# Optimization experiments

Hardware: AMD Instinct MI355X
Metric: run time of the kernel (lower is better)

The kernel has to match this reference:

```python
import jax, jax.numpy as jnp
import numpy as np

B, S, D, H = 128, 256, 256, 8   # graphs, nodes/graph, dim_h, heads
N = B * S
E = 524288
DH = D // H
BN_EPS = 1e-5

def _bn(v, g, b):
    # BatchNorm1d forward with batch statistics (biased var), eval-dropout model
    m = v.mean(0)
    var = v.var(0)
    return (v - m) * jax.lax.rsqrt(var + BN_EPS) * g + b

def setup_inputs() -> dict:
    key = jax.random.key(0)
    ks = jax.random.split(key, 40)
    x = jax.random.normal(ks[0], (N, D), jnp.float32)
    src = jax.random.randint(ks[1], (E,), 0, N)
    dst = (src // S) * S + jax.random.randint(ks[2], (E,), 0, S)  # intra-graph edges
    edge_index = jnp.stack([src, dst]).astype(jnp.int64)
    def lin(k, i, o):
        return (jax.random.normal(k, (i, o), jnp.float32) / np.float32(np.sqrt(i)))
    inp = {
        'x': x, 'edge_index': edge_index,
        'W_gcn': lin(ks[3], D, D), 'b_gcn': jnp.zeros((D,), jnp.float32),
        'W_gin1': lin(ks[4], D, D), 'b_gin1': jnp.zeros((D,), jnp.float32),
        'W_gin2': lin(ks[5], D, D), 'b_gin2': jnp.zeros((D,), jnp.float32),
        'g_kv': jnp.ones((D,), jnp.float32), 'be_kv': jnp.zeros((D,), jnp.float32),
        'Wq1': lin(ks[6], D, D), 'bq1': jnp.zeros((D,), jnp.float32),
        'Wq2': lin(ks[7], D, D), 'bq2': jnp.zeros((D,), jnp.float32),
        'Wq_a': lin(ks[8], D, D), 'bq_a': jnp.zeros((D,), jnp.float32),
        'Wk_a': lin(ks[9], D, D), 'bk_a': jnp.zeros((D,), jnp.float32),
        'Wv_a': lin(ks[10], D, D), 'bv_a': jnp.zeros((D,), jnp.float32),
        'Wo_a': lin(ks[11], D, D), 'bo_a': jnp.zeros((D,), jnp.float32),
        'g_attn': jnp.ones((D,), jnp.float32), 'be_attn': jnp.zeros((D,), jnp.float32),
        'Wf1': lin(ks[12], D, 2 * D), 'bf1': jnp.zeros((2 * D,), jnp.float32),
        'Wf2': lin(ks[13], 2 * D, D), 'bf2': jnp.zeros((D,), jnp.float32),
        'g2': jnp.ones((D,), jnp.float32), 'be2': jnp.zeros((D,), jnp.float32),
    }
    return inp

def _forward(x, edge_index,
             W_gcn, b_gcn, W_gin1, b_gin1, W_gin2, b_gin2, g_kv, be_kv,
             Wq1, bq1, Wq2, bq2,
             Wq_a, bq_a, Wk_a, bk_a, Wv_a, bv_a, Wo_a, bo_a, g_attn, be_attn,
             Wf1, bf1, Wf2, bf2, g2, be2):
    row, col = edge_index[0], edge_index[1]
    h_in1 = x

    # ---- expert 0: GCNConv (add self loops + symmetric norm) ----
    loops = jnp.arange(N, dtype=row.dtype)
    row2 = jnp.concatenate([row, loops])
    col2 = jnp.concatenate([col, loops])
    deg = jax.ops.segment_sum(jnp.ones_like(row2, jnp.float32), col2, num_segments=N)
    dinv = jnp.where(deg > 0, jax.lax.rsqrt(deg), 0.0)
    norm = dinv[row2] * dinv[col2]                     # [E+N]
    xw = x @ W_gcn                                      # [N, D]
    h_gcn = jax.ops.segment_sum(norm[:, None] * xw[row2], col2, num_segments=N) + b_gcn
    e0 = _bn(h_gcn, g_kv, be_kv)

    # ---- expert 1: GINConv (eps=0, sum aggregation, 2-layer MLP) ----
    agg = jax.ops.segment_sum(x[row], col, num_segments=N)
    h_gin = jax.nn.relu((x + agg) @ W_gin1 + b_gin1) @ W_gin2 + b_gin2
    e1 = _bn(h_gin, g_kv, be_kv)

    # ---- global expert normalization (torch .std -> unbiased) ----
    allo = jnp.concatenate([e0, e1], axis=0)
    gm = allo.mean()
    gs = jnp.std(allo, ddof=1)
    e0 = (e0 - gm) / (gs + 1e-8)
    e1 = (e1 - gm) / (gs + 1e-8)

    # ---- uniform routing & kv residual mix ----
    kv = 0.5 * e0 + 0.5 * e1 + 0.1 * h_in1              # [N, D]

    # ---- dense batching (equal-sized graphs -> pure reshape, full mask) ----
    q_dense = h_in1.reshape(B, S, D)
    kv_dense = kv.reshape(B, S, D)

    # ---- q projection MLP ----
    q_dense = jax.nn.relu(q_dense @ Wq1 + bq1) @ Wq2 + bq2

    # ---- multihead attention (batch_first, no padding) ----
    qh = (q_dense @ Wq_a + bq_a).reshape(B, S, H, DH)
    kh = (kv_dense @ Wk_a + bk_a).reshape(B, S, H, DH)
    vh = (kv_dense @ Wv_a + bv_a).reshape(B, S, H, DH)
    scores = jnp.einsum('bqhd,bkhd->bhqk', qh, kh) / np.float32(np.sqrt(DH))
    attn = jax.nn.softmax(scores, axis=-1)
    o = jnp.einsum('bhqk,bkhd->bqhd', attn, vh).reshape(B, S, D)
    h_attn = (o @ Wo_a + bo_a).reshape(N, D)

    # ---- residual + norm + FFN block ----
    h = _bn(h_in1 + h_attn, g_attn, be_attn)
    h_ff = jax.nn.relu(h @ Wf1 + bf1) @ Wf2 + bf2
    h = _bn(h + h_ff, g2, be2)
    return h

def reference(x, edge_index,
              W_gcn, b_gcn, W_gin1, b_gin1, W_gin2, b_gin2, g_kv, be_kv,
              Wq1, bq1, Wq2, bq2,
              Wq_a, bq_a, Wk_a, bk_a, Wv_a, bv_a, Wo_a, bo_a, g_attn, be_attn,
              Wf1, bf1, Wf2, bf2, g2, be2):
    return _forward(x, edge_index,
                    W_gcn, b_gcn, W_gin1, b_gin1, W_gin2, b_gin2, g_kv, be_kv,
                    Wq1, bq1, Wq2, bq2,
                    Wq_a, bq_a, Wk_a, bk_a, Wv_a, bv_a, Wo_a, bo_a, g_attn, be_attn,
                    Wf1, bf1, Wf2, bf2, g2, be2)
```

## Files before the change

### kernel.cpp

```cpp
#include <hip/hip_runtime.h>
#include <hip/hip_bf16.h>

typedef __hip_bfloat16 bf16;
typedef __attribute__((ext_vector_type(8))) short short8;
typedef __attribute__((ext_vector_type(4))) short short4v;
typedef __attribute__((ext_vector_type(4))) float f32x4;

#define N_ 32768
#define D_ 256
#define S_ 256
#define B_ 128
#define E_ 524288

static __device__ __forceinline__ f32x4 mfma16(short8 a, short8 b, f32x4 c) {
  return __builtin_amdgcn_mfma_f32_16x16x32_bf16(a, b, c, 0, 0, 0);
}
static __device__ __forceinline__ f32x4 fzero4() {
  f32x4 z; z[0] = 0.f; z[1] = 0.f; z[2] = 0.f; z[3] = 0.f; return z;
}
static __device__ __forceinline__ float bits2f(short s) {
  unsigned u = ((unsigned)(unsigned short)s) << 16;
  return __builtin_bit_cast(float, u);
}
static __device__ __forceinline__ short f2bits(float f) {
  bf16 b = __float2bfloat16(f);
  return __builtin_bit_cast(short, b);
}
static __device__ __forceinline__ float tof(float x) { return x; }
static __device__ __forceinline__ float tof(bf16 x) { return __bfloat162float(x); }

#define GLOAD_LDS16(G, L) __builtin_amdgcn_global_load_lds( \
    (const __attribute__((address_space(1))) void*)(G),     \
    (__attribute__((address_space(3))) void*)(L), 16, 0, 0)

template<int F>
__global__ __launch_bounds__(256)
void gemm_bt(const bf16* __restrict__ A, const bf16* __restrict__ Bt,
             const float* __restrict__ bias, const void* __restrict__ resid,
             float* __restrict__ Cf, bf16* __restrict__ Cb,
             float* __restrict__ Sp, float* __restrict__ SSp,
             int M, int Nc, int K, long bsA, long bsB, long bsC)
{
  __shared__ __align__(16) bf16 lA[128 * 32];
  __shared__ __align__(16) bf16 lB[128 * 32];
  __shared__ float sS[2][128], sSS[2][128];
  const int z = blockIdx.z;
  const bf16* Ab = A + (long)z * bsA;
  const bf16* Bb = Bt + (long)z * bsB;
  const int m0 = blockIdx.x * 128, n0 = blockIdx.y * 128;
  const int tid = threadIdx.x;
  const int lane = tid & 63;
  const int w = tid >> 6, wr = w >> 1, wc = w & 1;
  const int g = lane >> 4, r = lane & 15, ko = g * 8;
  const int srow = lane >> 2, skw = (lane & 3) * 8;

  f32x4 acc[4][4];
  for (int i = 0; i < 4; i++) for (int j = 0; j < 4; j++) acc[i][j] = fzero4();

  for (int k0 = 0; k0 < K; k0 += 32) {
    __syncthreads();
    for (int i = 0; i < 2; i++) {
      const int c = w * 2 + i;
      GLOAD_LDS16(Ab + (long)(m0 + c * 16 + srow) * K + k0 + skw, lA + c * 512);
      GLOAD_LDS16(Bb + (long)(n0 + c * 16 + srow) * K + k0 + skw, lB + c * 512);
    }
    __syncthreads();
    short8 af[4], bfv[4];
    for (int mi = 0; mi < 4; mi++)
      af[mi] = *(const short8*)&lA[(wr * 64 + mi * 16 + r) * 32 + ko];
    for (int ni = 0; ni < 4; ni++)
      bfv[ni] = *(const short8*)&lB[(wc * 64 + ni * 16 + r) * 32 + ko];
    for (int mi = 0; mi < 4; mi++)
      for (int ni = 0; ni < 4; ni++)
        acc[mi][ni] = mfma16(af[mi], bfv[ni], acc[mi][ni]);
  }

  float cs[4] = {0, 0, 0, 0}, css[4] = {0, 0, 0, 0};
  for (int mi = 0; mi < 4; mi++) for (int ni = 0; ni < 4; ni++) {
    const int row = m0 + wr * 64 + mi * 16 + g * 4;
    const int col = n0 + wc * 64 + ni * 16 + r;
    float bv = (F & 2) ? bias[col] : 0.0f;
    for (int j = 0; j < 4; j++) {
      long idx = (long)(row + j) * Nc + col;
      float v = acc[mi][ni][j] + bv;
      if (F & 4)  v += ((const float*)resid)[(long)z * bsC + idx];
      if (F & 64) v += bits2f(((const short*)resid)[(long)z * bsC + idx]);
      if (F & 1)  v = fmaxf(v, 0.0f);
      if (F & 32) { cs[ni] += v; css[ni] += v * v; }
      if (F & 8)  Cf[(long)z * bsC + idx] = v;
      if (F & 16) Cb[(long)z * bsC + idx] = __float2bfloat16(v);
    }
  }
  if (F & 32) {
    for (int ni = 0; ni < 4; ni++) {
      cs[ni]  += __shfl_xor(cs[ni], 16);  cs[ni]  += __shfl_xor(cs[ni], 32);
      css[ni] += __shfl_xor(css[ni], 16); css[ni] += __shfl_xor(css[ni], 32);
    }
    if (lane < 16) {
      for (int ni = 0; ni < 4; ni++) {
        sS[wr][wc * 64 + ni * 16 + lane]  = cs[ni];
        sSS[wr][wc * 64 + ni * 16 + lane] = css[ni];
      }
    }
    __syncthreads();
    if (tid < 128) {
      atomicAdd(&Sp[n0 + tid],  sS[0][tid] + sS[1][tid]);
      atomicAdd(&SSp[n0 + tid], sSS[0][tid] + sSS[1][tid]);
    }
  }
}

__global__ __launch_bounds__(256)
void attn_k(const bf16* __restrict__ qh, const bf16* __restrict__ kh,
            const bf16* __restrict__ vh, bf16* __restrict__ ob)
{
  const int h = blockIdx.x, b = blockIdx.y;
  const int tid = threadIdx.x, lane = tid & 63, w = tid >> 6;
  const int g = lane >> 4, r = lane & 15, ko = g * 8;
  __shared__ __align__(16) bf16 lK[256 * 40];
  __shared__ __align__(16) bf16 lV[32 * 264];
  __shared__ __align__(16) bf16 lP[4][16 * 264];

  for (int i = 0; i < 4; i++) {
    int s = tid + i * 256; int row = s >> 2, c = (s & 3) * 8;
    *(short8*)&lK[row * 40 + c] =
      *(const short8*)(kh + (long)(b * 256 + row) * 256 + h * 32 + c);
  }
  const bf16* vbp = vh + (long)b * 65536 + h * 32;
  for (int i = 0; i < 4; i++) {
    int q = tid + i * 256;
    int s = q >> 2, part = q & 3;
    short8 v = *(const short8*)(vbp + (long)s * 256 + part * 8);
    for (int j = 0; j < 8; j++)
      ((short*)lV)[(part * 8 + j) * 264 + s] = v[j];
  }
  __syncthreads();

  const float scale = 0.17677669529663687f;
  for (int mc = 0; mc < 4; mc++) {
    const long qrow = (long)b * 256 + w * 64 + mc * 16;
    short8 aq = *(const short8*)(qh + (qrow + r) * 256 + h * 32 + ko);
    f32x4 sc[16];
    for (int nc = 0; nc < 16; nc++) {
      short8 bk = *(const short8*)&lK[(nc * 16 + r) * 40 + ko];
      sc[nc] = mfma16(aq, bk, fzero4());
    }
    float rsum[4];
    for (int j = 0; j < 4; j++) {
      float mx = -3.4e38f;
      for (int nc = 0; nc < 16; nc++) mx = fmaxf(mx, sc[nc][j]);
      mx = fmaxf(mx, __shfl_xor(mx, 1));
      mx = fmaxf(mx, __shfl_xor(mx, 2));
      mx = fmaxf(mx, __shfl_xor(mx, 4));
      mx = fmaxf(mx, __shfl_xor(mx, 8));
      float sum = 0.f;
      for (int nc = 0; nc < 16; nc++) {
        float p = __expf((sc[nc][j] - mx) * scale);
        sc[nc][j] = p; sum += p;
      }
      sum += __shfl_xor(sum, 1); sum += __shfl_xor(sum, 2);
      sum += __shfl_xor(sum, 4); sum += __shfl_xor(sum, 8);
      rsum[j] = sum;
      for (int nc = 0; nc < 16; nc++)
        lP[w][(g * 4 + j) * 264 + nc * 16 + r] = __float2bfloat16(sc[nc][j]);
    }
    f32x4 oa[2]; oa[0] = fzero4(); oa[1] = fzero4();
    for (int kc = 0; kc < 8; kc++) {
      short8 ap = *(const short8*)&lP[w][r * 264 + kc * 32 + ko];
      for (int n = 0; n < 2; n++) {
        short8 bv = *(const short8*)&lV[(n * 16 + r) * 264 + kc * 32 + ko];
        oa[n] = mfma16(ap, bv, oa[n]);
      }
    }
    for (int n = 0; n < 2; n++) for (int j = 0; j < 4; j++) {
      float v = oa[n][j] / rsum[j];
      ob[(qrow + g * 4 + j) * 256 + h * 32 + n * 16 + r] = __float2bfloat16(v);
    }
  }
}

template<typename TIN>
__global__ __launch_bounds__(256)
void transpose_cast_k(const TIN* __restrict__ in, bf16* __restrict__ out,
                      int in_rs, int out_rs, long zhi, long out_zs)
{
  __shared__ float tile[32][33];
  const int z = blockIdx.z;
  const long ioff = (long)z * zhi;
  const long ooff = (long)z * out_zs;
  const int tx = threadIdx.x, ty = threadIdx.y;
  const int c = blockIdx.x * 32 + tx;
  const int rb = blockIdx.y * 32;
  for (int i = 0; i < 4; i++)
    tile[ty + i * 8][tx] = tof(in[ioff + (long)(rb + ty + i * 8) * in_rs + c]);
  __syncthreads();
  const int oc = rb + tx;
  const int orb = blockIdx.x * 32;
  for (int i = 0; i < 4; i++)
    out[ooff + (long)(orb + ty + i * 8) * out_rs + oc] =
      __float2bfloat16(tile[tx][ty + i * 8]);
}

__global__ __launch_bounds__(256)
void w9t_k(const float* w0, const float* w1, const float* w2, const float* w3,
           const float* w4, const float* w5, const float* w6, const float* w7,
           const float* w8, bf16* __restrict__ out)
{
  __shared__ float tile[32][33];
  const float* srcs[9] = {w0, w1, w2, w3, w4, w5, w6, w7, w8};
  const int wi = blockIdx.z;
  const float* in = srcs[wi];
  bf16* o = out + (long)wi * 65536;
  const int tx = threadIdx.x, ty = threadIdx.y;
  const int c = blockIdx.x * 32 + tx;
  const int rb = blockIdx.y * 32;
  for (int i = 0; i < 4; i++)
    tile[ty + i * 8][tx] = in[(rb + ty + i * 8) * 256 + c];
  __syncthreads();
  const int oc = rb + tx;
  const int orb = blockIdx.x * 32;
  for (int i = 0; i < 4; i++)
    o[(orb + ty + i * 8) * 256 + oc] = __float2bfloat16(tile[tx][ty + i * 8]);
}

__global__ __launch_bounds__(256)
void cast4_k(const float* __restrict__ in, bf16* __restrict__ out)
{
  long i = ((long)blockIdx.x * 256 + threadIdx.x) * 4;
  float4 v = *(const float4*)(in + i);
  short4v o;
  o[0] = f2bits(v.x); o[1] = f2bits(v.y); o[2] = f2bits(v.z); o[3] = f2bits(v.w);
  *(short4v*)(out + i) = o;
}

__global__ __launch_bounds__(256)
void edge_cnt_k(const int* __restrict__ ei, unsigned* __restrict__ cnt)
{
  int e = blockIdx.x * 256 + threadIdx.x;
  int src = ei[e], dst = ei[E_ + e];
  long idx = ((long)(src >> 8) * 256 + (dst & 255)) * 256 + (src & 255);
  atomicAdd(&cnt[idx >> 1], 1u << ((idx & 1) * 16));
}

__global__ __launch_bounds__(256)
void deg_k(const unsigned* __restrict__ cnt, float* __restrict__ dinv)
{
  int rid = blockIdx.x * 16 + (threadIdx.x >> 4);
  int l16 = threadIdx.x & 15;
  const uint4* rp = (const uint4*)(cnt + (long)rid * 128);
  unsigned s = 0;
  for (int i = 0; i < 2; i++) {
    uint4 v = rp[l16 + i * 16];
    s += (v.x & 0xFFFF) + (v.x >> 16) + (v.y & 0xFFFF) + (v.y >> 16)
       + (v.z & 0xFFFF) + (v.z >> 16) + (v.w & 0xFFFF) + (v.w >> 16);
  }
  s += __shfl_xor(s, 1); s += __shfl_xor(s, 2);
  s += __shfl_xor(s, 4); s += __shfl_xor(s, 8);
  if (l16 == 0) dinv[rid] = rsqrtf((float)s + 1.0f);
}

__global__ __launch_bounds__(256)
void adj_derive_k(const unsigned* __restrict__ cnt, const float* __restrict__ dinv,
                  bf16* __restrict__ gin, bf16* __restrict__ gcn)
{
  long i = ((long)blockIdx.x * 256 + threadIdx.x) * 4;
  uint2 cp = *(const uint2*)(cnt + (i >> 1));
  float cv[4] = {(float)(cp.x & 0xFFFF), (float)(cp.x >> 16),
                 (float)(cp.y & 0xFFFF), (float)(cp.y >> 16)};
  long row = i >> 8;
  int g = (int)(row >> 8), dst = (int)(row & 255);
  int src0 = (int)(i & 255);
  float dd = dinv[row];
  const float* ds = dinv + (long)g * 256 + src0;
  short4v oi, oc;
  for (int j = 0; j < 4; j++) {
    float gv = cv[j] * dd * ds[j];
    if (src0 + j == dst) gv += dd * dd;
    oi[j] = f2bits(cv[j]);
    oc[j] = f2bits(gv);
  }
  *(short4v*)(gin + i) = oi;
  *(short4v*)(gcn + i) = oc;
}

__global__ __launch_bounds__(256)
void expert_stats_k(const float* __restrict__ S0, const float* __restrict__ SS0,
                    const float* __restrict__ S1, const float* __restrict__ SS1,
                    const float* __restrict__ gkv, const float* __restrict__ bkv,
                    float* __restrict__ kA, float* __restrict__ kB,
                    float* __restrict__ kC)
{
  const int d = threadIdx.x;
  const float invN = 1.0f / 32768.0f;
  float m0 = S0[d] * invN, v0 = SS0[d] * invN - m0 * m0;
  float a0 = gkv[d] * rsqrtf(v0 + 1e-5f), c0 = bkv[d] - m0 * a0;
  float m1 = S1[d] * invN, v1 = SS1[d] * invN - m1 * m1;
  float a1 = gkv[d] * rsqrtf(v1 + 1e-5f), c1 = bkv[d] - m1 * a1;
  float gsum = a0 * S0[d] + 32768.0f * c0 + a1 * S1[d] + 32768.0f * c1;
  float gss  = a0 * a0 * SS0[d] + 2.0f * a0 * c0 * S0[d] + 32768.0f * c0 * c0
             + a1 * a1 * SS1[d] + 2.0f * a1 * c1 * S1[d] + 32768.0f * c1 * c1;
  __shared__ float r1[256], r2[256];
  r1[d] = gsum; r2[d] = gss;
  __syncthreads();
  for (int s = 128; s > 0; s >>= 1) {
    if (d < s) { r1[d] += r1[d + s]; r2[d] += r2[d + s]; }
    __syncthreads();
  }
  const float cntall = 16777216.0f;
  float tg = r1[0], tss = r2[0];
  float gm = tg / cntall;
  float var = (tss - tg * tg / cntall) / (cntall - 1.0f);
  float gs = sqrtf(fmaxf(var, 0.f)) + 1e-8f;
  kA[d] = 0.5f * a0 / gs;
  kB[d] = 0.5f * a1 / gs;
  kC[d] = 0.5f * (c0 + c1 - 2.0f * gm) / gs;
}

__global__ __launch_bounds__(256)
void kv_mix_k(const bf16* __restrict__ hgcn, const bf16* __restrict__ hgin,
              const bf16* __restrict__ xb, const float* __restrict__ kA,
              const float* __restrict__ kB, const float* __restrict__ kC,
              bf16* __restrict__ kv)
{
  long i = ((long)blockIdx.x * 256 + threadIdx.x) * 8;
  int d0 = (int)(i & 255);
  short8 a = *(const short8*)(hgcn + i);
  short8 b = *(const short8*)(hgin + i);
  short8 c = *(const short8*)(xb + i);
  short8 o;
  for (int j = 0; j < 8; j++) {
    int d = d0 + j;
    float v = kA[d] * bits2f(a[j]) + kB[d] * bits2f(b[j]) + kC[d] + 0.1f * bits2f(c[j]);
    o[j] = f2bits(v);
  }
  *(short8*)(kv + i) = o;
}

template<int MODE>
__global__ __launch_bounds__(256)
void bn_apply_k(const bf16* __restrict__ in, const float* __restrict__ S,
                const float* __restrict__ SSq, const float* __restrict__ gg,
                const float* __restrict__ bb, float* __restrict__ outf,
                bf16* __restrict__ outb)
{
  long i = ((long)blockIdx.x * 256 + threadIdx.x) * 8;
  int d0 = (int)(i & 255);
  short8 v = *(const short8*)(in + i);
  const float invN = 1.0f / 32768.0f;
  float4 o0, o1; short8 o8;
  for (int j = 0; j < 8; j++) {
    int d = d0 + j;
    float m = S[d] * invN;
    float var = SSq[d] * invN - m * m;
    float a = gg[d] * rsqrtf(var + 1e-5f);
    float c = bb[d] - m * a;
    float o = a * bits2f(v[j]) + c;
    if (MODE & 1) { if (j < 4) (&o0.x)[j] = o; else (&o1.x)[j - 4] = o; }
    if (MODE & 2) o8[j] = f2bits(o);
  }
  if (MODE & 1) { *(float4*)(outf + i) = o0; *(float4*)(outf + i + 4) = o1; }
  if (MODE & 2) *(short8*)(outb + i) = o8;
}

static constexpr size_t OFF_S0 = 0, OFF_SS0 = 1024, OFF_S1 = 2048, OFF_SS1 = 3072;
static constexpr size_t OFF_S2 = 4096, OFF_SS2 = 5120, OFF_S3 = 6144, OFF_SS3 = 7168;
static constexpr size_t OFF_KA = 8192, OFF_KB = 9216, OFF_KC = 10240;
static constexpr size_t OFF_CNT = 16384;
static constexpr size_t CNT_BYTES = (size_t)B_ * S_ * S_ * 2;
static constexpr size_t ZERO_BYTES = OFF_CNT + CNT_BYTES;
static constexpr size_t OFF_DINV = ZERO_BYTES;
static constexpr size_t OFF_W = OFF_DINV + 131072;
static constexpr size_t NDB2 = (size_t)N_ * D_ * 2;
static constexpr size_t OFF_ADJGINB = OFF_W + 1703936;
static constexpr size_t OFF_ADJGCNB = OFF_ADJGINB + NDB2;
static constexpr size_t OFF_XB   = OFF_ADJGCNB + NDB2;
static constexpr size_t OFF_XT   = OFF_XB + NDB2;
static constexpr size_t OFF_XWB  = OFF_XT + NDB2;
static constexpr size_t OFF_XWT  = OFF_XWB + NDB2;
static constexpr size_t OFF_KV   = OFF_XWT + NDB2;
static constexpr size_t OFF_HGCN = OFF_KV + NDB2;
static constexpr size_t OFF_HGIN = OFF_HGCN + NDB2;

extern "C" void kernel_launch(void* const* d_in, const int* in_sizes, int n_in,
                              void* d_out, int out_size, void* d_ws, size_t ws_size,
                              hipStream_t stream)
{
  (void)in_sizes; (void)n_in; (void)out_size; (void)ws_size;
  const float* x      = (const float*)d_in[0];
  const int*   ei     = (const int*)d_in[1];
  const float* W_gcn  = (const float*)d_in[2];
  const float* b_gcn  = (const float*)d_in[3];
  const float* W_gin1 = (const float*)d_in[4];
  const float* b_gin1 = (const float*)d_in[5];
  const float* W_gin2 = (const float*)d_in[6];
  const float* b_gin2 = (const float*)d_in[7];
  const float* g_kv   = (const float*)d_in[8];
  const float* be_kv  = (const float*)d_in[9];
  const float* Wq1    = (const float*)d_in[10];
  const float* bq1    = (const float*)d_in[11];
  const float* Wq2    = (const float*)d_in[12];
  const float* bq2    = (const float*)d_in[13];
  const float* Wq_a   = (const float*)d_in[14];
  const float* bq_a   = (const float*)d_in[15];
  const float* Wk_a   = (const float*)d_in[16];
  const float* bk_a   = (const float*)d_in[17];
  const float* Wv_a   = (const float*)d_in[18];
  const float* bv_a   = (const float*)d_in[19];
  const float* Wo_a   = (const float*)d_in[20];
  const float* bo_a   = (const float*)d_in[21];
  const float* g_attn = (const float*)d_in[22];
  const float* be_attn= (const float*)d_in[23];
  const float* Wf1    = (const float*)d_in[24];
  const float* bf1    = (const float*)d_in[25];
  const float* Wf2    = (const float*)d_in[26];
  const float* bf2    = (const float*)d_in[27];
  const float* g2     = (const float*)d_in[28];
  const float* be2    = (const float*)d_in[29];

  char* ws = (char*)d_ws;
  float* S0  = (float*)(ws + OFF_S0);  float* SS0 = (float*)(ws + OFF_SS0);
  float* S1  = (float*)(ws + OFF_S1);  float* SS1 = (float*)(ws + OFF_SS1);
  float* S2  = (float*)(ws + OFF_S2);  float* SS2 = (float*)(ws + OFF_SS2);
  float* S3  = (float*)(ws + OFF_S3);  float* SS3 = (float*)(ws + OFF_SS3);
  float* kA  = (float*)(ws + OFF_KA);  float* kB  = (float*)(ws + OFF_KB);
  float* kC  = (float*)(ws + OFF_KC);
  unsigned* cntA = (unsigned*)(ws + OFF_CNT);
  float* dinv = (float*)(ws + OFF_DINV);
  bf16* wT = (bf16*)(ws + OFF_W);
  bf16 *WgcnT = wT,            *Wgin1T = wT + 65536,  *Wgin2T = wT + 131072;
  bf16 *Wq1T  = wT + 196608,   *Wq2T   = wT + 262144, *WqaT   = wT + 327680;
  bf16 *WkaT  = wT + 393216,   *WvaT   = wT + 458752, *WoaT   = wT + 524288;
  bf16 *Wf1T  = wT + 589824,   *Wf2T   = wT + 720896;
  bf16* adjGINb = (bf16*)(ws + OFF_ADJGINB);
  bf16* adjGCNb = (bf16*)(ws + OFF_ADJGCNB);
  bf16* xb    = (bf16*)(ws + OFF_XB);
  bf16* xT    = (bf16*)(ws + OFF_XT);
  bf16* xw_bf = (bf16*)(ws + OFF_XWB);
  bf16* xwT   = (bf16*)(ws + OFF_XWT);
  bf16* kv_bf = (bf16*)(ws + OFF_KV);
  bf16* hgcnb = (bf16*)(ws + OFF_HGCN);
  bf16* hginb = (bf16*)(ws + OFF_HGIN);
  bf16* gin_in = xw_bf;
  bf16* gin_h  = adjGCNb;
  bf16* qhb    = adjGCNb;
  bf16* khb    = adjGINb;
  bf16* q1b    = xT;
  bf16* qb     = xw_bf;
  bf16* vhb    = hgcnb;
  bf16* ob     = hginb;
  bf16* tbufb  = (bf16*)(ws + OFF_CNT);
  bf16* hb     = xb;
  bf16* f1b    = (bf16*)(ws + OFF_XWT);
  bf16* t2b    = adjGCNb;
  float* outp  = (float*)d_out;

  hipMemsetAsync(d_ws, 0, ZERO_BYTES, stream);

  dim3 tb(32, 8);
  w9t_k<<<dim3(8, 8, 9), tb, 0, stream>>>(W_gcn, W_gin1, W_gin2, Wq1, Wq2,
                                          Wq_a, Wk_a, Wv_a, Wo_a, wT);
  transpose_cast_k<float><<<dim3(16, 8, 1), tb, 0, stream>>>(Wf1, Wf1T, 512, 256, 0, 0);
  transpose_cast_k<float><<<dim3(8, 16, 1), tb, 0, stream>>>(Wf2, Wf2T, 256, 512, 0, 0);
  cast4_k<<<8192, 256, 0, stream>>>(x, xb);
  transpose_cast_k<float><<<dim3(8, 8, 128), tb, 0, stream>>>(x, xT, 256, 256, 65536, 65536);
  edge_cnt_k<<<2048, 256, 0, stream>>>(ei, cntA);
  deg_k<<<2048, 256, 0, stream>>>(cntA, dinv);
  adj_derive_k<<<8192, 256, 0, stream>>>(cntA, dinv, adjGINb, adjGCNb);
  gemm_bt<16><<<dim3(256, 2, 1), 256, 0, stream>>>(xb, WgcnT, nullptr, nullptr,
      nullptr, xw_bf, nullptr, nullptr, N_, 256, 256, 0, 0, 0);
  transpose_cast_k<bf16><<<dim3(8, 8, 128), tb, 0, stream>>>(xw_bf, xwT, 256, 256, 65536, 65536);
  gemm_bt<50><<<dim3(2, 2, 128), 256, 0, stream>>>(adjGCNb, xwT, b_gcn, nullptr,
      nullptr, hgcnb, S0, SS0, 256, 256, 256, 65536, 65536, 65536);
  gemm_bt<80><<<dim3(2, 2, 128), 256, 0, stream>>>(adjGINb, xT, nullptr, xb,
      nullptr, gin_in, nullptr, nullptr, 256, 256, 256, 65536, 65536, 65536);
  gemm_bt<19><<<dim3(256, 2, 1), 256, 0, stream>>>(gin_in, Wgin1T, b_gin1, nullptr,
      nullptr, gin_h, nullptr, nullptr, N_, 256, 256, 0, 0, 0);
  gemm_bt<50><<<dim3(256, 2, 1), 256, 0, stream>>>(gin_h, Wgin2T, b_gin2, nullptr,
      nullptr, hginb, S1, SS1, N_, 256, 256, 0, 0, 0);
  expert_stats_k<<<1, 256, 0, stream>>>(S0, SS0, S1, SS1, g_kv, be_kv, kA, kB, kC);
  kv_mix_k<<<4096, 256, 0, stream>>>(hgcnb, hginb, xb, kA, kB, kC, kv_bf);
  gemm_bt<19><<<dim3(256, 2, 1), 256, 0, stream>>>(xb, Wq1T, bq1, nullptr,
      nullptr, q1b, nullptr, nullptr, N_, 256, 256, 0, 0, 0);
  gemm_bt<18><<<dim3(256, 2, 1), 256, 0, stream>>>(q1b, Wq2T, bq2, nullptr,
      nullptr, qb, nullptr, nullptr, N_, 256, 256, 0, 0, 0);
  gemm_bt<18><<<dim3(256, 2, 1), 256, 0, stream>>>(qb, WqaT, bq_a, nullptr,
      nullptr, qhb, nullptr, nullptr, N_, 256, 256, 0, 0, 0);
  gemm_bt<18><<<dim3(256, 2, 1), 256, 0, stream>>>(kv_bf, WkaT, bk_a, nullptr,
      nullptr, khb, nullptr, nullptr, N_, 256, 256, 0, 0, 0);
  gemm_bt<18><<<dim3(256, 2, 1), 256, 0, stream>>>(kv_bf, WvaT, bv_a, nullptr,
      nullptr, vhb, nullptr, nullptr, N_, 256, 256, 0, 0, 0);
  attn_k<<<dim3(8, 128), 256, 0, stream>>>(qhb, khb, vhb, ob);
  gemm_bt<114><<<dim3(256, 2, 1), 256, 0, stream>>>(ob, WoaT, bo_a, xb,
      nullptr, tbufb, S2, SS2, N_, 256, 256, 0, 0, 0);
  bn_apply_k<2><<<4096, 256, 0, stream>>>(tbufb, S2, SS2, g_attn, be_attn, nullptr, hb);
  gemm_bt<19><<<dim3(256, 4, 1), 256, 0, stream>>>(hb, Wf1T, bf1, nullptr,
      nullptr, f1b, nullptr, nullptr, N_, 512, 256, 0, 0, 0);
  gemm_bt<114><<<dim3(256, 2, 1), 256, 0, stream>>>(f1b, Wf2T, bf2, hb,
      nullptr, t2b, S3, SS3, N_, 256, 512, 0, 0, 0);
  bn_apply_k<1><<<4096, 256, 0, stream>>>(t2b, S3, SS3, g2, be2, outp, nullptr);
}
```

Measured before the change: 354.5 us.

## Reassociate GCN product to skip transpose; rework attention with swizzled LDS and bpermute

The GCN expert now computes (A·X)·W instead of A·(X·W). It reuses the already transposed xT, which removes one dense GEMM-to-transpose round trip, and the workspace buffers are remapped to match. The attention kernel computes S^T via swapped MFMA operands and stores K and V in XOR-swizzled LDS without padding. It normalises probabilities before the PV product and passes them between lanes with ds_bpermute instead of an LDS staging buffer. Launch bounds now request 4 blocks per CU. The cost is more permute instructions and a change in rounding order for the GCN branch.

```diff
diff --git a/kernel.cpp b/kernel.cpp
--- a/kernel.cpp
+++ b/kernel.cpp
@@ -5,6 +5,7 @@
 typedef __attribute__((ext_vector_type(8))) short short8;
 typedef __attribute__((ext_vector_type(4))) short short4v;
 typedef __attribute__((ext_vector_type(4))) float f32x4;
+typedef __attribute__((ext_vector_type(4))) int i32x4;
 
 #define N_ 32768
 #define D_ 256
@@ -110,72 +111,107 @@
   }
 }
 
-__global__ __launch_bounds__(256)
+__global__ __launch_bounds__(256, 4)
 void attn_k(const bf16* __restrict__ qh, const bf16* __restrict__ kh,
             const bf16* __restrict__ vh, bf16* __restrict__ ob)
 {
   const int h = blockIdx.x, b = blockIdx.y;
   const int tid = threadIdx.x, lane = tid & 63, w = tid >> 6;
   const int g = lane >> 4, r = lane & 15, ko = g * 8;
-  __shared__ __align__(16) bf16 lK[256 * 40];
-  __shared__ __align__(16) bf16 lV[32 * 264];
-  __shared__ __align__(16) bf16 lP[4][16 * 264];
+  __shared__ __align__(16) bf16 lK[256 * 32];
+  __shared__ __align__(16) bf16 lV[32 * 256];
+  char* lKc = (char*)lK;
+  char* lVc = (char*)lV;
 
   for (int i = 0; i < 4; i++) {
-    int s = tid + i * 256; int row = s >> 2, c = (s & 3) * 8;
-    *(short8*)&lK[row * 40 + c] =
-      *(const short8*)(kh + (long)(b * 256 + row) * 256 + h * 32 + c);
-  }
-  const bf16* vbp = vh + (long)b * 65536 + h * 32;
+    int c = tid + i * 256;
+    int row = c >> 2, p4 = c & 3;
+    short8 v = *(const short8*)(kh + (long)(b * 256 + row) * 256 + h * 32 + p4 * 8);
+    *(short8*)(lKc + ((row * 64 + p4 * 16) ^ ((row & 7) << 4))) = v;
+  }
   for (int i = 0; i < 4; i++) {
-    int q = tid + i * 256;
-    int s = q >> 2, part = q & 3;
-    short8 v = *(const short8*)(vbp + (long)s * 256 + part * 8);
-    for (int j = 0; j < 8; j++)
-      ((short*)lV)[(part * 8 + j) * 264 + s] = v[j];
+    int c = tid + i * 256;
+    int s = c >> 2, part = c & 3;
+    short8 v = *(const short8*)(vh + (long)(b * 256 + s) * 256 + h * 32 + part * 8);
+    for (int j = 0; j < 8; j++) {
+      int dh = part * 8 + j;
+      int sw = ((dh & 7) ^ ((dh >> 3) << 1)) & 7;
+      *(short*)(lVc + ((dh * 512 + s * 2) ^ (sw << 4))) = v[j];
+    }
   }
   __syncthreads();
 
   const float scale = 0.17677669529663687f;
+  const int idx0 = (((lane >> 4) & 1) * 32 + r) * 4;
+  const int idx1 = idx0 + 64;
+  const bool selhi = lane >= 32;
+
   for (int mc = 0; mc < 4; mc++) {
-    const long qrow = (long)b * 256 + w * 64 + mc * 16;
-    short8 aq = *(const short8*)(qh + (qrow + r) * 256 + h * 32 + ko);
+    const long qbase = (long)b * 256 + w * 64 + mc * 16;
+    short8 qf = *(const short8*)(qh + (qbase + r) * 256 + h * 32 + ko);
     f32x4 sc[16];
+    #pragma unroll
     for (int nc = 0; nc < 16; nc++) {
-      short8 bk = *(const short8*)&lK[(nc * 16 + r) * 40 + ko];
-      sc[nc] = mfma16(aq, bk, fzero4());
-    }
-    float rsum[4];
-    for (int j = 0; j < 4; j++) {
-      float mx = -3.4e38f;
-      for (int nc = 0; nc < 16; nc++) mx = fmaxf(mx, sc[nc][j]);
-      mx = fmaxf(mx, __shfl_xor(mx, 1));
-      mx = fmaxf(mx, __shfl_xor(mx, 2));
-      mx = fmaxf(mx, __shfl_xor(mx, 4));
-      mx = fmaxf(mx, __shfl_xor(mx, 8));
-      float sum = 0.f;
-      for (int nc = 0; nc < 16; nc++) {
+      int row = nc * 16 + r;
+      short8 kf = *(const short8*)(lKc + ((row * 64 + g * 16) ^ ((r & 7) << 4)));
+      sc[nc] = mfma16(kf, qf, fzero4());
+    }
+    f32x4 m4 = sc[0];
+    #pragma unroll
+    for (int nc = 1; nc < 16; nc++)
+      for (int j = 0; j < 4; j++) m4[j] = fmaxf(m4[j], sc[nc][j]);
+    float mx = fmaxf(fmaxf(m4[0], m4[1]), fmaxf(m4[2], m4[3]));
+    mx = fmaxf(mx, __shfl_xor(mx, 16));
+    mx = fmaxf(mx, __shfl_xor(mx, 32));
+    f32x4 s4 = fzero4();
+    #pragma unroll
+    for (int nc = 0; nc < 16; nc++)
+      for (int j = 0; j < 4; j++) {
         float p = __expf((sc[nc][j] - mx) * scale);
-        sc[nc][j] = p; sum += p;
+        sc[nc][j] = p; s4[j] += p;
       }
-      sum += __shfl_xor(sum, 1); sum += __shfl_xor(sum, 2);
-      sum += __shfl_xor(sum, 4); sum += __shfl_xor(sum, 8);
-      rsum[j] = sum;
-      for (int nc = 0; nc < 16; nc++)
-        lP[w][(g * 4 + j) * 264 + nc * 16 + r] = __float2bfloat16(sc[nc][j]);
-    }
+    float sum = s4[0] + s4[1] + s4[2] + s4[3];
+    sum += __shfl_xor(sum, 16);
+    sum += __shfl_xor(sum, 32);
+    const float invs = 1.0f / sum;
+    int pk[16][2];
+    #pragma unroll
+    for (int nc = 0; nc < 16; nc++)
+      for (int hh = 0; hh < 2; hh++) {
+        unsigned lo = (unsigned short)f2bits(sc[nc][2 * hh] * invs);
+        unsigned hi = (unsigned short)f2bits(sc[nc][2 * hh + 1] * invs);
+        pk[nc][hh] = (int)((hi << 16) | lo);
+      }
     f32x4 oa[2]; oa[0] = fzero4(); oa[1] = fzero4();
+    #pragma unroll
     for (int kc = 0; kc < 8; kc++) {
-      short8 ap = *(const short8*)&lP[w][r * 264 + kc * 32 + ko];
+      int A0 = __builtin_amdgcn_ds_bpermute(idx0, pk[2 * kc][0]);
+      int A1 = __builtin_amdgcn_ds_bpermute(idx0, pk[2 * kc][1]);
+      int B0 = __builtin_amdgcn_ds_bpermute(idx0, pk[2 * kc + 1][0]);
+      int B1 = __builtin_amdgcn_ds_bpermute(idx0, pk[2 * kc + 1][1]);
+      int C0 = __builtin_amdgcn_ds_bpermute(idx1, pk[2 * kc][0]);
+      int C1 = __builtin_amdgcn_ds_bpermute(idx1, pk[2 * kc][1]);
+      int D0 = __builtin_amdgcn_ds_bpermute(idx1, pk[2 * kc + 1][0]);
+      int D1 = __builtin_amdgcn_ds_bpermute(idx1, pk[2 * kc + 1][1]);
+      i32x4 av;
+      av[0] = selhi ? B0 : A0;
+      av[1] = selhi ? B1 : A1;
+      av[2] = selhi ? D0 : C0;
+      av[3] = selhi ? D1 : C1;
+      short8 af = __builtin_bit_cast(short8, av);
+      #pragma unroll
       for (int n = 0; n < 2; n++) {
-        short8 bv = *(const short8*)&lV[(n * 16 + r) * 264 + kc * 32 + ko];
-        oa[n] = mfma16(ap, bv, oa[n]);
+        int dh = n * 16 + r;
+        int sw = ((dh & 7) ^ ((dh >> 3) << 1)) & 7;
+        short8 bv = *(const short8*)(lVc + ((dh * 512 + kc * 64 + g * 16) ^ (sw << 4)));
+        oa[n] = mfma16(af, bv, oa[n]);
       }
     }
-    for (int n = 0; n < 2; n++) for (int j = 0; j < 4; j++) {
-      float v = oa[n][j] / rsum[j];
-      ob[(qrow + g * 4 + j) * 256 + h * 32 + n * 16 + r] = __float2bfloat16(v);
-    }
+    #pragma unroll
+    for (int n = 0; n < 2; n++)
+      for (int j = 0; j < 4; j++)
+        ob[(qbase + g * 4 + j) * 256 + h * 32 + n * 16 + r] =
+          __float2bfloat16(oa[n][j]);
   }
 }
 
@@ -375,9 +411,9 @@
 static constexpr size_t OFF_ADJGCNB = OFF_ADJGINB + NDB2;
 static constexpr size_t OFF_XB   = OFF_ADJGCNB + NDB2;
 static constexpr size_t OFF_XT   = OFF_XB + NDB2;
-static constexpr size_t OFF_XWB  = OFF_XT + NDB2;
-static constexpr size_t OFF_XWT  = OFF_XWB + NDB2;
-static constexpr size_t OFF_KV   = OFF_XWT + NDB2;
+static constexpr size_t OFF_AGG  = OFF_XT + NDB2;
+static constexpr size_t OFF_GIN  = OFF_AGG + NDB2;
+static constexpr size_t OFF_KV   = OFF_GIN + NDB2;
 static constexpr size_t OFF_HGCN = OFF_KV + NDB2;
 static constexpr size_t OFF_HGIN = OFF_HGCN + NDB2;
 
@@ -435,23 +471,22 @@
   bf16* adjGCNb = (bf16*)(ws + OFF_ADJGCNB);
   bf16* xb    = (bf16*)(ws + OFF_XB);
   bf16* xT    = (bf16*)(ws + OFF_XT);
-  bf16* xw_bf = (bf16*)(ws + OFF_XWB);
-  bf16* xwT   = (bf16*)(ws + OFF_XWT);
+  bf16* aggb  = (bf16*)(ws + OFF_AGG);
+  bf16* gin_in= (bf16*)(ws + OFF_GIN);
   bf16* kv_bf = (bf16*)(ws + OFF_KV);
   bf16* hgcnb = (bf16*)(ws + OFF_HGCN);
   bf16* hginb = (bf16*)(ws + OFF_HGIN);
-  bf16* gin_in = xw_bf;
   bf16* gin_h  = adjGCNb;
-  bf16* qhb    = adjGCNb;
-  bf16* khb    = adjGINb;
+  bf16* qhb    = adjGINb;
   bf16* q1b    = xT;
-  bf16* qb     = xw_bf;
+  bf16* qb     = aggb;
+  bf16* khb    = gin_in;
   bf16* vhb    = hgcnb;
   bf16* ob     = hginb;
   bf16* tbufb  = (bf16*)(ws + OFF_CNT);
   bf16* hb     = xb;
-  bf16* f1b    = (bf16*)(ws + OFF_XWT);
-  bf16* t2b    = adjGCNb;
+  bf16* f1b    = adjGINb;
+  bf16* t2b    = gin_in;
   float* outp  = (float*)d_out;
 
   hipMemsetAsync(d_ws, 0, ZERO_BYTES, stream);
@@ -466,13 +501,12 @@
   edge_cnt_k<<<2048, 256, 0, stream>>>(ei, cntA);
   deg_k<<<2048, 256, 0, stream>>>(cntA, dinv);
   adj_derive_k<<<8192, 256, 0, stream>>>(cntA, dinv, adjGINb, adjGCNb);
-  gemm_bt<16><<<dim3(256, 2, 1), 256, 0, stream>>>(xb, WgcnT, nullptr, nullptr,
-      nullptr, xw_bf, nullptr, nullptr, N_, 256, 256, 0, 0, 0);
-  transpose_cast_k<bf16><<<dim3(8, 8, 128), tb, 0, stream>>>(xw_bf, xwT, 256, 256, 65536, 65536);
-  gemm_bt<50><<<dim3(2, 2, 128), 256, 0, stream>>>(adjGCNb, xwT, b_gcn, nullptr,
-      nullptr, hgcnb, S0, SS0, 256, 256, 256, 65536, 65536, 65536);
+  gemm_bt<16><<<dim3(2, 2, 128), 256, 0, stream>>>(adjGCNb, xT, nullptr, nullptr,
+      nullptr, aggb, nullptr, nullptr, 256, 256, 256, 65536, 65536, 65536);
   gemm_bt<80><<<dim3(2, 2, 128), 256, 0, stream>>>(adjGINb, xT, nullptr, xb,
       nullptr, gin_in, nullptr, nullptr, 256, 256, 256, 65536, 65536, 65536);
+  gemm_bt<50><<<dim3(256, 2, 1), 256, 0, stream>>>(aggb, WgcnT, b_gcn, nullptr,
+      nullptr, hgcnb, S0, SS0, N_, 256, 256, 0, 0, 0);
   gemm_bt<19><<<dim3(256, 2, 1), 256, 0, stream>>>(gin_in, Wgin1T, b_gin1, nullptr,
       nullptr, gin_h, nullptr, nullptr, N_, 256, 256, 0, 0, 0);
   gemm_bt<50><<<dim3(256, 2, 1), 256, 0, stream>>>(gin_h, Wgin2T, b_gin2, nullptr,
```

Result: slower. 425.5 us (+20.0%).
